# Performance work log

Hardware: AMD Instinct MI355X
Metric: run time of the kernel (lower is better)

Reference implementation:

```python
import jax, jax.numpy as jnp
import numpy as np
from jax import lax

WIN = 9
PAD = WIN // 2


def _box_sum(x):
    # x: [B,1,H,W]; all-ones WINxWIN conv, stride 1, pad PAD -> same spatial size
    k = jnp.ones((1, 1, WIN, WIN), dtype=x.dtype)
    return lax.conv_general_dilated(
        x, k, window_strides=(1, 1), padding=[(PAD, PAD), (PAD, PAD)],
        dimension_numbers=("NCHW", "OIHW", "NCHW"))


def setup_inputs() -> dict:
    key = jax.random.key(0)
    k1, k2 = jax.random.split(key)
    B, C, H, W = 32, 1, 512, 512
    y_true = jax.random.uniform(k1, (B, C, H, W), dtype=jnp.float32)
    y_pred = jax.random.uniform(k2, (B, C, H, W), dtype=jnp.float32)
    return {"y_true": y_true, "y_pred": y_pred}


def reference(y_true, y_pred):
    Ii, Ji = y_true, y_pred
    win_size = float(WIN * WIN)
    I_sum = _box_sum(Ii)
    J_sum = _box_sum(Ji)
    I2_sum = _box_sum(Ii * Ii)
    J2_sum = _box_sum(Ji * Ji)
    IJ_sum = _box_sum(Ii * Ji)
    u_I = I_sum / win_size
    u_J = J_sum / win_size
    cross = IJ_sum - u_J * I_sum - u_I * J_sum + u_I * u_J * win_size
    I_var = I2_sum - 2.0 * u_I * I_sum + u_I * u_I * win_size
    J_var = J2_sum - 2.0 * u_J * J_sum + u_J * u_J * win_size
    cc = cross * cross / (I_var * J_var + 1e-05)
    return -jnp.mean(cc)
```

## Files before the change

kernel.cpp:

```cpp
#include <hip/hip_runtime.h>


#define BATCH   32
#define IMH     512
#define IMW     512
#define SH      28
#define NSTRIP  19
#define NROUND  4
#define NBLOCKS (BATCH * NSTRIP)
#define LROW    520
#define AROWS   36
#define LDSZ    (AROWS * LROW)

__global__ __launch_bounds__(256, 2) void ncc_main(const float* __restrict__ I,
                                                   const float* __restrict__ J,
                                                   float* __restrict__ acc_ws,
                                                   unsigned* __restrict__ cnt_ws,
                                                   float* __restrict__ out) {
    __shared__ __align__(16) float lds[LDSZ];
    __shared__ float wsum[4];

    const int t    = threadIdx.x;
    const int lane = t & 63;
    const int w    = t >> 6;
    const int arr  = w >> 1;
    const int h    = w & 1;
    const int s    = blockIdx.x;
    const int b    = blockIdx.y;
    const int r0   = s * SH;
    const float inv81 = 1.0f / 81.0f;

    const float* Ib = I + (size_t)b * IMH * IMW;
    const float* Jb = J + (size_t)b * IMH * IMW;
    const float* src = arr ? Jb : Ib;

    auto lrow = [](int buf, int a, int q) {
        return ((buf * 2 + a) * 9 + q) * LROW;
    };

    auto dma_round = [&](int R, int buf) {
#pragma unroll
        for (int q = 0; q < 9; ++q) {
            const int ri = r0 - 4 + R * 9 + q;
            float* ldst = &lds[lrow(buf, arr, q) + 4 + h * 256];
            if ((unsigned)ri < (unsigned)IMH) {
                const float* gsrc = src + (size_t)ri * IMW + h * 256 + lane * 4;
                __builtin_amdgcn_global_load_lds(
                    (const __attribute__((address_space(1))) void*)gsrc,
                    (__attribute__((address_space(3))) void*)ldst,
                    16, 0, 0);
            } else {
                *(float4*)(ldst + lane * 4) = make_float4(0.f, 0.f, 0.f, 0.f);
            }
        }
    };

    for (int idx = t; idx < AROWS * 8; idx += 256) {
        const int arow = idx >> 3;
        const int k    = idx & 7;
        lds[arow * LROW + ((k < 4) ? k : (512 + k))] = 0.f;
    }

    dma_round(0, 0);
    __syncthreads();

    float2 ring[9][5];
#pragma unroll
    for (int j = 0; j < 9; ++j)
#pragma unroll
        for (int q = 0; q < 5; ++q) ring[j][q] = make_float2(0.f, 0.f);

    float2 V[5];
#pragma unroll
    for (int q = 0; q < 5; ++q) V[q] = make_float2(0.f, 0.f);

    float2 acc = make_float2(0.f, 0.f);

#pragma unroll 1
    for (int R = 0; R < NROUND; ++R) {
        if (R + 1 < NROUND) dma_round(R + 1, (R + 1) & 1);

        const int baseI = lrow(R & 1, 0, 0) + 2 * t;
        const int baseJ = lrow(R & 1, 1, 0) + 2 * t;

#pragma unroll
        for (int j = 0; j < 9; ++j) {
            const int i = R * 9 + j;

            float vI[10], vJ[10];
#pragma unroll
            for (int k = 0; k < 5; ++k) {
                const float2 a = *(const float2*)&lds[baseI + j * LROW + 2 * k];
                const float2 c = *(const float2*)&lds[baseJ + j * LROW + 2 * k];
                vI[2 * k] = a.x; vI[2 * k + 1] = a.y;
                vJ[2 * k] = c.x; vJ[2 * k + 1] = c.y;
            }

            float sI = 0.f, sJ = 0.f, sII = 0.f, sJJ = 0.f, sIJ = 0.f;
#pragma unroll
            for (int m = 0; m < 9; ++m) {
                sI  += vI[m];
                sJ  += vJ[m];
                sII += vI[m] * vI[m];
                sJJ += vJ[m] * vJ[m];
                sIJ += vI[m] * vJ[m];
            }
            const float i0 = vI[0], j0 = vJ[0], i9 = vI[9], j9 = vJ[9];
            float2 Hn[5];
            Hn[0] = make_float2(sI,  sI  + i9      - i0);
            Hn[1] = make_float2(sJ,  sJ  + j9      - j0);
            Hn[2] = make_float2(sII, sII + i9 * i9 - i0 * i0);
            Hn[3] = make_float2(sJJ, sJJ + j9 * j9 - j0 * j0);
            Hn[4] = make_float2(sIJ, sIJ + i9 * j9 - i0 * j0);

#pragma unroll
            for (int q = 0; q < 5; ++q) {
                const float2 old = ring[j][q];
                ring[j][q] = Hn[q];
                V[q].x += Hn[q].x - old.x;
                V[q].y += Hn[q].y - old.y;
            }

            if (i >= 8 && (r0 + i - 8) < IMH) {
                {
                    const float aI = V[0].x, aJ = V[1].x;
                    const float cross = V[4].x - aI * aJ * inv81;
                    const float iv    = V[2].x - aI * aI * inv81;
                    const float jv    = V[3].x - aJ * aJ * inv81;
                    acc.x += cross * cross *
                             __builtin_amdgcn_rcpf(iv * jv + 1e-5f);
                }
                {
                    const float aI = V[0].y, aJ = V[1].y;
                    const float cross = V[4].y - aI * aJ * inv81;
                    const float iv    = V[2].y - aI * aI * inv81;
                    const float jv    = V[3].y - aJ * aJ * inv81;
                    acc.y += cross * cross *
                             __builtin_amdgcn_rcpf(iv * jv + 1e-5f);
                }
            }
        }
        __syncthreads();
    }

    float sum = acc.x + acc.y;
#pragma unroll
    for (int off = 32; off > 0; off >>= 1) sum += __shfl_down(sum, off, 64);

    if ((t & 63) == 0) wsum[t >> 6] = sum;
    __syncthreads();
    if (t == 0) {
        const float bsum = wsum[0] + wsum[1] + wsum[2] + wsum[3];
        atomicAdd(acc_ws, bsum);
        __threadfence();
        const unsigned old = atomicAdd(cnt_ws, 1u);
        if (old == (unsigned)(NBLOCKS - 1)) {
            const float total = atomicAdd(acc_ws, 0.0f);
            out[0] = -total / 8388608.0f;
        }
    }
}

extern "C" void kernel_launch(void* const* d_in, const int* in_sizes, int n_in,
                              void* d_out, int out_size, void* d_ws, size_t ws_size,
                              hipStream_t stream) {
    const float* I = (const float*)d_in[0];
    const float* J = (const float*)d_in[1];
    float* acc_ws  = (float*)d_ws;
    unsigned* cnt  = (unsigned*)d_ws + 1;
    float* out     = (float*)d_out;

    hipMemsetAsync(d_ws, 0, 2 * sizeof(float), stream);

    dim3 grid(NSTRIP, BATCH);
    ncc_main<<<grid, 256, 0, stream>>>(I, J, acc_ws, cnt, out);
}
```

Before: 125.0 us.

## Replace LDS double buffer with register-staged prefetch to raise occupancy

New measurement: 155.6 us. 24.5% more time.

```diff
diff --git a/kernel.cpp b/kernel.cpp
--- a/kernel.cpp
+++ b/kernel.cpp
@@ -9,10 +9,10 @@
 #define NROUND  4
 #define NBLOCKS (BATCH * NSTRIP)
 #define LROW    520
-#define AROWS   36
+#define AROWS   18
 #define LDSZ    (AROWS * LROW)
 
-__global__ __launch_bounds__(256, 2) void ncc_main(const float* __restrict__ I,
+__global__ __launch_bounds__(256, 3) void ncc_main(const float* __restrict__ I,
                                                    const float* __restrict__ J,
                                                    float* __restrict__ acc_ws,
                                                    unsigned* __restrict__ cnt_ws,
@@ -20,48 +20,46 @@
     __shared__ __align__(16) float lds[LDSZ];
     __shared__ float wsum[4];
 
-    const int t    = threadIdx.x;
-    const int lane = t & 63;
-    const int w    = t >> 6;
-    const int arr  = w >> 1;
-    const int h    = w & 1;
-    const int s    = blockIdx.x;
-    const int b    = blockIdx.y;
-    const int r0   = s * SH;
+    const int t   = threadIdx.x;
+    const int s   = blockIdx.x;
+    const int b   = blockIdx.y;
+    const int r0  = s * SH;
     const float inv81 = 1.0f / 81.0f;
 
     const float* Ib = I + (size_t)b * IMH * IMW;
     const float* Jb = J + (size_t)b * IMH * IMW;
+
+    const int arr  = t >> 7;
+    const int col  = 4 * (t & 127);
     const float* src = arr ? Jb : Ib;
+    float* const dstbase = &lds[arr * 9 * LROW + 4 + col];
 
-    auto lrow = [](int buf, int a, int q) {
-        return ((buf * 2 + a) * 9 + q) * LROW;
-    };
+    float4 stg[9];
+    const float4 zero4 = make_float4(0.f, 0.f, 0.f, 0.f);
 
-    auto dma_round = [&](int R, int buf) {
+    auto load_round = [&](int R) {
 #pragma unroll
         for (int q = 0; q < 9; ++q) {
             const int ri = r0 - 4 + R * 9 + q;
-            float* ldst = &lds[lrow(buf, arr, q) + 4 + h * 256];
-            if ((unsigned)ri < (unsigned)IMH) {
-                const float* gsrc = src + (size_t)ri * IMW + h * 256 + lane * 4;
-                __builtin_amdgcn_global_load_lds(
-                    (const __attribute__((address_space(1))) void*)gsrc,
-                    (__attribute__((address_space(3))) void*)ldst,
-                    16, 0, 0);
-            } else {
-                *(float4*)(ldst + lane * 4) = make_float4(0.f, 0.f, 0.f, 0.f);
-            }
+            stg[q] = ((unsigned)ri < (unsigned)IMH)
+                         ? *(const float4*)(src + (size_t)ri * IMW + col)
+                         : zero4;
         }
     };
+    auto write_round = [&]() {
+#pragma unroll
+        for (int q = 0; q < 9; ++q)
+            *(float4*)(dstbase + q * LROW) = stg[q];
+    };
 
-    for (int idx = t; idx < AROWS * 8; idx += 256) {
-        const int arow = idx >> 3;
-        const int k    = idx & 7;
+    if (t < AROWS * 8) {
+        const int arow = t >> 3;
+        const int k    = t & 7;
         lds[arow * LROW + ((k < 4) ? k : (512 + k))] = 0.f;
     }
 
-    dma_round(0, 0);
+    load_round(0);
+    write_round();
     __syncthreads();
 
     float2 ring[9][5];
@@ -78,10 +76,10 @@
 
 #pragma unroll 1
     for (int R = 0; R < NROUND; ++R) {
-        if (R + 1 < NROUND) dma_round(R + 1, (R + 1) & 1);
+        if (R + 1 < NROUND) load_round(R + 1);
 
-        const int baseI = lrow(R & 1, 0, 0) + 2 * t;
-        const int baseJ = lrow(R & 1, 1, 0) + 2 * t;
+        const int baseI = 2 * t;
+        const int baseJ = 9 * LROW + 2 * t;
 
 #pragma unroll
         for (int j = 0; j < 9; ++j) {
@@ -140,7 +138,12 @@
                 }
             }
         }
-        __syncthreads();
+
+        if (R + 1 < NROUND) {
+            __syncthreads();
+            write_round();
+            __syncthreads();
+        }
     }
 
     float sum = acc.x + acc.y;
```

## Single-buffer LDS with smaller strips to raise occupancy to four blocks per CU

Applied to the files above, without the earlier changes.

Result: slower. 164.3 us (+31.4%).

```diff
diff --git a/kernel.cpp b/kernel.cpp
--- a/kernel.cpp
+++ b/kernel.cpp
@@ -4,15 +4,15 @@
 #define BATCH   32
 #define IMH     512
 #define IMW     512
-#define SH      28
-#define NSTRIP  19
-#define NROUND  4
+#define SH      19
+#define NSTRIP  27
+#define NROUND  3
 #define NBLOCKS (BATCH * NSTRIP)
 #define LROW    520
-#define AROWS   36
+#define AROWS   18
 #define LDSZ    (AROWS * LROW)
 
-__global__ __launch_bounds__(256, 2) void ncc_main(const float* __restrict__ I,
+__global__ __launch_bounds__(256, 4) void ncc_main(const float* __restrict__ I,
                                                    const float* __restrict__ J,
                                                    float* __restrict__ acc_ws,
                                                    unsigned* __restrict__ cnt_ws,
@@ -30,38 +30,30 @@
     const int r0   = s * SH;
     const float inv81 = 1.0f / 81.0f;
 
-    const float* Ib = I + (size_t)b * IMH * IMW;
-    const float* Jb = J + (size_t)b * IMH * IMW;
+    const float* Ib  = I + (size_t)b * IMH * IMW;
+    const float* Jb  = J + (size_t)b * IMH * IMW;
     const float* src = arr ? Jb : Ib;
+    float* const abase = &lds[arr * 9 * LROW];
 
-    auto lrow = [](int buf, int a, int q) {
-        return ((buf * 2 + a) * 9 + q) * LROW;
-    };
+#pragma unroll
+    for (int q = 0; q < 9; ++q) {
+        const int ri = r0 - 4 + q;
+        float* ldst = abase + q * LROW + 4 + h * 256;
+        if ((unsigned)ri < (unsigned)IMH) {
+            const float* gsrc = src + (size_t)ri * IMW + h * 256 + lane * 4;
+            __builtin_amdgcn_global_load_lds(
+                (const __attribute__((address_space(1))) void*)gsrc,
+                (__attribute__((address_space(3))) void*)ldst, 16, 0, 0);
+        } else {
+            *(float4*)(ldst + lane * 4) = make_float4(0.f, 0.f, 0.f, 0.f);
+        }
+    }
 
-    auto dma_round = [&](int R, int buf) {
-#pragma unroll
-        for (int q = 0; q < 9; ++q) {
-            const int ri = r0 - 4 + R * 9 + q;
-            float* ldst = &lds[lrow(buf, arr, q) + 4 + h * 256];
-            if ((unsigned)ri < (unsigned)IMH) {
-                const float* gsrc = src + (size_t)ri * IMW + h * 256 + lane * 4;
-                __builtin_amdgcn_global_load_lds(
-                    (const __attribute__((address_space(1))) void*)gsrc,
-                    (__attribute__((address_space(3))) void*)ldst,
-                    16, 0, 0);
-            } else {
-                *(float4*)(ldst + lane * 4) = make_float4(0.f, 0.f, 0.f, 0.f);
-            }
-        }
-    };
-
-    for (int idx = t; idx < AROWS * 8; idx += 256) {
-        const int arow = idx >> 3;
-        const int k    = idx & 7;
+    if (t < AROWS * 8) {
+        const int arow = t >> 3;
+        const int k    = t & 7;
         lds[arow * LROW + ((k < 4) ? k : (512 + k))] = 0.f;
     }
-
-    dma_round(0, 0);
     __syncthreads();
 
     float2 ring[9][5];
@@ -76,13 +68,11 @@
 
     float2 acc = make_float2(0.f, 0.f);
 
+    const int baseI = 2 * t;
+    const int baseJ = 9 * LROW + 2 * t;
+
 #pragma unroll 1
     for (int R = 0; R < NROUND; ++R) {
-        if (R + 1 < NROUND) dma_round(R + 1, (R + 1) & 1);
-
-        const int baseI = lrow(R & 1, 0, 0) + 2 * t;
-        const int baseJ = lrow(R & 1, 1, 0) + 2 * t;
-
 #pragma unroll
         for (int j = 0; j < 9; ++j) {
             const int i = R * 9 + j;
@@ -140,7 +130,24 @@
                 }
             }
         }
-        __syncthreads();
+
+        if (R + 1 < NROUND) {
+            __syncthreads();
+#pragma unroll
+            for (int q = 0; q < 9; ++q) {
+                const int ri = r0 - 4 + (R + 1) * 9 + q;
+                float* ldst = abase + q * LROW + 4 + h * 256;
+                if ((unsigned)ri < (unsigned)IMH) {
+                    const float* gsrc = src + (size_t)ri * IMW + h * 256 + lane * 4;
+                    __builtin_amdgcn_global_load_lds(
+                        (const __attribute__((address_space(1))) void*)gsrc,
+                        (__attribute__((address_space(3))) void*)ldst, 16, 0, 0);
+                } else {
+                    *(float4*)(ldst + lane * 4) = make_float4(0.f, 0.f, 0.f, 0.f);
+                }
+            }
+            __syncthreads();
+        }
     }
 
     float sum = acc.x + acc.y;
```
